# Performance work log

Measured on AMD Instinct MI355X. Metric: run time of the kernel, lower is better.

Reference implementation:

```python
import jax, jax.numpy as jnp
import numpy as np

B, T, N, H = 256, 128, 512, 128  # batch, timesteps, input_size (driving series), hidden


def setup_inputs() -> dict:
    key = jax.random.key(0)
    ks = jax.random.split(key, 7)
    p = lambda k, shape: (jax.random.normal(k, shape, dtype=jnp.float32) * 0.05)
    return {
        "X": jax.random.normal(ks[0], (B, T, N), dtype=jnp.float32),
        # attention linear: in_features = 2H + T, out_features = 1 (stored as a vector + scalar bias)
        "attn_w": p(ks[1], (2 * H + T,)),
        "attn_b": p(ks[2], ()),
        # LSTM cell params, PyTorch layout/gate order (i, f, g, o)
        "w_ih": p(ks[3], (4 * H, N)),
        "w_hh": p(ks[4], (4 * H, H)),
        "b_ih": p(ks[5], (4 * H,)),
        "b_hh": p(ks[6], (4 * H,)),
    }


def reference(X, attn_w, attn_b, w_ih, w_hh, b_ih, b_hh):
    Bn, Tn, Nn = X.shape
    Hh = w_hh.shape[1]
    # split the single attention weight row into the h / s / X-row pieces of the concat
    w_h, w_s, w_x = attn_w[:Hh], attn_w[Hh:2 * Hh], attn_w[2 * Hh:]
    Xp = jnp.swapaxes(X, 1, 2)            # [B, N, T]  (X.permute(0,2,1))
    x_score = Xp @ w_x                    # [B, N], time-invariant part of attention logits

    def step(carry, x_t):                 # x_t: [B, N] = X[:, t, :]
        h, c = carry
        # logits[b,i] = w_h.h[b] + w_s.c[b] + w_x.Xp[b,i] + b  (== Linear on the concat)
        score = x_score + (h @ w_h + c @ w_s + attn_b)[:, None]   # [B, N]
        alpha = jax.nn.softmax(score, axis=1)
        x_tilde = alpha * x_t                                      # [B, N]
        gates = x_tilde @ w_ih.T + h @ w_hh.T + b_ih + b_hh        # [B, 4H]
        i, f, g, o = jnp.split(gates, 4, axis=1)
        c_new = jax.nn.sigmoid(f) * c + jax.nn.sigmoid(i) * jnp.tanh(g)
        h_new = jax.nn.sigmoid(o) * jnp.tanh(c_new)
        return (h_new, c_new), (x_tilde, h_new)

    h0 = jnp.zeros((Bn, Hh), X.dtype)
    (_, _), (Xt, Xe) = jax.lax.scan(step, (h0, h0), jnp.swapaxes(X, 0, 1))
    # scan stacks along time -> [T, B, .]; return [B, T, .]
    return jnp.swapaxes(Xt, 0, 1), jnp.swapaxes(Xe, 0, 1)
```

## Files before the change

### kernel.cpp

```cpp
#include <hip/hip_runtime.h>
#include <hip/hip_bf16.h>

#define Bb 256
#define Tt 128
#define Nn 512
#define Hh 128

typedef __attribute__((ext_vector_type(4))) float floatx4;
typedef __attribute__((ext_vector_type(8))) short short8;

__device__ __forceinline__ unsigned short f2bf(float f) {
  unsigned u = __float_as_uint(f);
  u += 0x7fffu + ((u >> 16) & 1u);
  return (unsigned short)(u >> 16);
}

__device__ __forceinline__ float sigmoid_fast(float x) {
  return __builtin_amdgcn_rcpf(1.f + __expf(-x));
}
__device__ __forceinline__ float tanh_fast(float x) {
  float e = __expf(2.f * x);
  return 1.f - 2.f * __builtin_amdgcn_rcpf(e + 1.f);
}

__device__ __forceinline__ void lds_barrier() {
  asm volatile("s_waitcnt lgkmcnt(0)" ::: "memory");
  __builtin_amdgcn_s_barrier();
  asm volatile("" ::: "memory");
}

__global__ void prep_kernel(const float* __restrict__ w_ih,
                            const float* __restrict__ b_ih,
                            const float* __restrict__ b_hh,
                            unsigned short* __restrict__ wb,
                            float* __restrict__ bias) {
  int i = blockIdx.x * 256 + threadIdx.x;
  if (i < 4 * Hh * Nn) wb[i] = f2bf(w_ih[i]);
  if (i < 4 * Hh) bias[i] = b_ih[i] + b_hh[i];
}

__global__ __launch_bounds__(512) void alpha_kernel(const float* __restrict__ X,
                                                    const float* __restrict__ attn_w,
                                                    float* __restrict__ alpha) {
  int b = blockIdx.x;
  int n = threadIdx.x;
  const float* Xb = X + (size_t)b * Tt * Nn + n;
  float acc = 0.f;
#pragma unroll 8
  for (int t = 0; t < Tt; ++t)
    acc = fmaf(Xb[(size_t)t * Nn], attn_w[2 * Hh + t], acc);

  __shared__ float red[512];
  red[n] = acc;
  __syncthreads();
  for (int s = 256; s > 0; s >>= 1) {
    if (n < s) red[n] = fmaxf(red[n], red[n + s]);
    __syncthreads();
  }
  float m = red[0];
  __syncthreads();
  float e = __expf(acc - m);
  red[n] = e;
  __syncthreads();
  for (int s = 256; s > 0; s >>= 1) {
    if (n < s) red[n] += red[n + s];
    __syncthreads();
  }
  alpha[(size_t)b * Nn + n] = e / red[0];
}

__global__ __launch_bounds__(256) void scale_kernel(const float* __restrict__ X,
                                                    const float* __restrict__ alpha,
                                                    float* __restrict__ Xt,
                                                    unsigned short* __restrict__ xtb) {
  size_t i = (size_t)blockIdx.x * 256 + threadIdx.x;
  size_t e = i * 4;
  int n = (int)(e & (Nn - 1));
  int brow = (int)(e >> 9);
  int b = brow >> 7;
  float4 x = ((const float4*)X)[i];
  float4 a = *(const float4*)(alpha + (size_t)b * Nn + n);
  float4 y;
  y.x = x.x * a.x; y.y = x.y * a.y; y.z = x.z * a.z; y.w = x.w * a.w;
  ((float4*)Xt)[i] = y;
  ushort4 u;
  u.x = f2bf(y.x); u.y = f2bf(y.y); u.z = f2bf(y.z); u.w = f2bf(y.w);
  ((ushort4*)xtb)[i] = u;
}

#define GBK 64
#define LDK 72

__global__ __launch_bounds__(256) void gemm_bt(const unsigned short* __restrict__ A,
                                               const unsigned short* __restrict__ Bw,
                                               const float* __restrict__ bias,
                                               float* __restrict__ C) {
  __shared__ __align__(16) unsigned short As[128 * LDK];
  __shared__ __align__(16) unsigned short Bs[128 * LDK];
  const int K = 512, NO = 512;
  int tid = threadIdx.x;
  int lane = tid & 63;
  int wave = tid >> 6;
  int wm = wave & 1, wn = wave >> 1;
  int l15 = lane & 15;
  int quad = lane >> 4;
  int mtile = blockIdx.x, ntile = blockIdx.y;

  floatx4 acc[4][4];
#pragma unroll
  for (int i = 0; i < 4; ++i)
#pragma unroll
    for (int j = 0; j < 4; ++j) acc[i][j] = (floatx4){0.f, 0.f, 0.f, 0.f};

  const size_t abase = (size_t)mtile * 128 * K;
  const size_t bbase = (size_t)ntile * 128 * K;

  for (int kb = 0; kb < K; kb += GBK) {
#pragma unroll
    for (int s = 0; s < 4; ++s) {
      int idx = s * 256 + tid;
      int r = idx >> 3;
      int c = (idx & 7) * 8;
      uint4 va = *(const uint4*)(A + abase + (size_t)r * K + kb + c);
      *(uint4*)(&As[r * LDK + c]) = va;
      uint4 vb = *(const uint4*)(Bw + bbase + (size_t)r * K + kb + c);
      *(uint4*)(&Bs[r * LDK + c]) = vb;
    }
    __syncthreads();
#pragma unroll
    for (int ks = 0; ks < GBK; ks += 32) {
      int kof = ks + quad * 8;
      short8 af[4], bf[4];
#pragma unroll
      for (int i = 0; i < 4; ++i)
        af[i] = *(const short8*)(&As[(wm * 64 + i * 16 + l15) * LDK + kof]);
#pragma unroll
      for (int j = 0; j < 4; ++j)
        bf[j] = *(const short8*)(&Bs[(wn * 64 + j * 16 + l15) * LDK + kof]);
#pragma unroll
      for (int i = 0; i < 4; ++i)
#pragma unroll
        for (int j = 0; j < 4; ++j)
          acc[i][j] = __builtin_amdgcn_mfma_f32_16x16x32_bf16(af[i], bf[j], acc[i][j], 0, 0, 0);
    }
    __syncthreads();
  }

  int m0 = mtile * 128 + wm * 64;
  int n0 = ntile * 128 + wn * 64;
#pragma unroll
  for (int j = 0; j < 4; ++j) {
    int col = n0 + j * 16 + l15;
    float bsum = bias[col];
#pragma unroll
    for (int i = 0; i < 4; ++i) {
      int row = m0 + i * 16 + quad * 4;
#pragma unroll
      for (int r = 0; r < 4; ++r)
        C[(size_t)(row + r) * NO + col] = acc[i][j][r] + bsum;
    }
  }
}

__global__ __launch_bounds__(256, 1) void lstm_kernel(const float* __restrict__ G,
                                                      const float* __restrict__ w_hh,
                                                      float* __restrict__ Xe) {
  int b = blockIdx.x;
  int tid = threadIdx.x;
  int w = tid >> 6;
  int lane = tid & 63;
  int l15 = lane & 15;
  int quad = lane >> 4;

  short8 bfr[8][4];
#pragma unroll
  for (int f = 0; f < 8; ++f) {
    int ftype = f >> 1, half = f & 1;
    int n = ftype * 128 + w * 32 + half * 16 + l15;
    const float* src = w_hh + (size_t)n * 128;
#pragma unroll
    for (int kf = 0; kf < 4; ++kf) {
      int k0 = kf * 32 + quad * 8;
      float4 lo = *(const float4*)(src + k0);
      float4 hi = *(const float4*)(src + k0 + 4);
      short8 v;
      v[0] = (short)f2bf(lo.x); v[1] = (short)f2bf(lo.y);
      v[2] = (short)f2bf(lo.z); v[3] = (short)f2bf(lo.w);
      v[4] = (short)f2bf(hi.x); v[5] = (short)f2bf(hi.y);
      v[6] = (short)f2bf(hi.z); v[7] = (short)f2bf(hi.w);
      bfr[f][kf] = v;
    }
  }

  __shared__ __align__(16) unsigned short h_sh[2][128];
  if (tid < 128) h_sh[0][tid] = 0;
  __syncthreads();

  const float* Gb = G + (size_t)b * Tt * 512;
  float* Xeb = Xe + (size_t)b * Tt * Hh;

  int goff[8];
#pragma unroll
  for (int f = 0; f < 8; ++f) {
    int ftype = f >> 1, half = f & 1;
    goff[f] = ftype * 128 + w * 32 + half * 16 + l15;
  }

  float gcur[8], gnext[8];
#pragma unroll
  for (int f = 0; f < 8; ++f) gcur[f] = Gb[goff[f]];
#pragma unroll
  for (int f = 0; f < 8; ++f) gnext[f] = Gb[512 + goff[f]];

  float c0 = 0.f, c1 = 0.f;
  int j0 = w * 32 + l15;

  for (int t = 0; t < Tt; ++t) {
    int cur = t & 1;
    const unsigned short* hp = h_sh[cur];
    short8 af[4];
#pragma unroll
    for (int kf = 0; kf < 4; ++kf)
      af[kf] = *(const short8*)(hp + kf * 32 + quad * 8);

    floatx4 acc[8];
#pragma unroll
    for (int f = 0; f < 8; ++f)
      acc[f] = (floatx4){gcur[f], gcur[f], gcur[f], gcur[f]};

#pragma unroll
    for (int f = 0; f < 8; ++f) gcur[f] = gnext[f];
    if (t + 2 < Tt) {
      const float* Gt2 = Gb + (size_t)(t + 2) * 512;
#pragma unroll
      for (int f = 0; f < 8; ++f) gnext[f] = Gt2[goff[f]];
    }

#pragma unroll
    for (int kf = 0; kf < 4; ++kf)
#pragma unroll
      for (int f = 0; f < 8; ++f)
        acc[f] = __builtin_amdgcn_mfma_f32_16x16x32_bf16(af[kf], bfr[f][kf], acc[f], 0, 0, 0);

    float si0 = sigmoid_fast(acc[0][0]), si1 = sigmoid_fast(acc[1][0]);
    float sf0 = sigmoid_fast(acc[2][0]), sf1 = sigmoid_fast(acc[3][0]);
    float tg0 = tanh_fast(acc[4][0]),    tg1 = tanh_fast(acc[5][0]);
    float so0 = sigmoid_fast(acc[6][0]), so1 = sigmoid_fast(acc[7][0]);

    c0 = sf0 * c0 + si0 * tg0;
    c1 = sf1 * c1 + si1 * tg1;
    float hv0 = so0 * tanh_fast(c0);
    float hv1 = so1 * tanh_fast(c1);

    if (quad == 0) {
      float* xo = Xeb + (size_t)t * Hh;
      xo[j0] = hv0;
      xo[j0 + 16] = hv1;
      unsigned short* hn = h_sh[cur ^ 1];
      hn[j0] = f2bf(hv0);
      hn[j0 + 16] = f2bf(hv1);
    }
    lds_barrier();
  }
}

extern "C" void kernel_launch(void* const* d_in, const int* in_sizes, int n_in,
                              void* d_out, int out_size, void* d_ws, size_t ws_size,
                              hipStream_t stream) {
  const float* X      = (const float*)d_in[0];
  const float* attn_w = (const float*)d_in[1];
  const float* w_ih   = (const float*)d_in[3];
  const float* w_hh   = (const float*)d_in[4];
  const float* b_ih   = (const float*)d_in[5];
  const float* b_hh   = (const float*)d_in[6];

  float* Xt = (float*)d_out;
  float* Xe = (float*)d_out + (size_t)Bb * Tt * Nn;

  char* ws = (char*)d_ws;
  float*          alpha = (float*)(ws);
  float*          bias  = (float*)(ws + 524288);
  unsigned short* wb    = (unsigned short*)(ws + 526336);
  unsigned short* xtb   = (unsigned short*)(ws + 1050624);
  float*          G     = (float*)(ws + 34605056);

  prep_kernel<<<dim3(1024), dim3(256), 0, stream>>>(w_ih, b_ih, b_hh, wb, bias);
  alpha_kernel<<<dim3(Bb), dim3(512), 0, stream>>>(X, attn_w, alpha);
  scale_kernel<<<dim3(16384), dim3(256), 0, stream>>>(X, alpha, Xt, xtb);
  gemm_bt<<<dim3(256, 4), dim3(256), 0, stream>>>(xtb, wb, bias, G);
  lstm_kernel<<<dim3(Bb), dim3(512 / 2), 0, stream>>>(G, w_hh, Xe);
}
```

Before: 290.0 us.

## Use async global-to-LDS swizzled loads in GEMM and widen LSTM to 8 waves

The bf16 GEMM now stages tiles with global_load_lds direct-to-LDS transfers into an unpadded, XOR-swizzled layout instead of register round-trip copies into padded rows, aiming to cut load instructions and LDS bank conflicts. The LSTM recurrence kernel is widened from 256 to 512 threads, so each wave owns 16 hidden units and 4 gate MFMAs per step instead of 8. This shortens each wave's serial per-step chain and splits the weight registers across more waves. The cost is a barrier across more waves every timestep.

```diff
diff --git a/kernel.cpp b/kernel.cpp
--- a/kernel.cpp
+++ b/kernel.cpp
@@ -27,6 +27,12 @@
   asm volatile("s_waitcnt lgkmcnt(0)" ::: "memory");
   __builtin_amdgcn_s_barrier();
   asm volatile("" ::: "memory");
+}
+
+__device__ __forceinline__ void async_load16(const void* g, void* lds) {
+  __builtin_amdgcn_global_load_lds(
+      (const __attribute__((address_space(1))) unsigned int*)g,
+      (__attribute__((address_space(3))) unsigned int*)lds, 16, 0, 0);
 }
 
 __global__ void prep_kernel(const float* __restrict__ w_ih,
@@ -89,14 +95,13 @@
 }
 
 #define GBK 64
-#define LDK 72
 
 __global__ __launch_bounds__(256) void gemm_bt(const unsigned short* __restrict__ A,
                                                const unsigned short* __restrict__ Bw,
                                                const float* __restrict__ bias,
                                                float* __restrict__ C) {
-  __shared__ __align__(16) unsigned short As[128 * LDK];
-  __shared__ __align__(16) unsigned short Bs[128 * LDK];
+  __shared__ __align__(16) unsigned short As[128 * 64];
+  __shared__ __align__(16) unsigned short Bs[128 * 64];
   const int K = 512, NO = 512;
   int tid = threadIdx.x;
   int lane = tid & 63;
@@ -112,31 +117,31 @@
 #pragma unroll
     for (int j = 0; j < 4; ++j) acc[i][j] = (floatx4){0.f, 0.f, 0.f, 0.f};
 
-  const size_t abase = (size_t)mtile * 128 * K;
-  const size_t bbase = (size_t)ntile * 128 * K;
+  int lr = lane >> 3;
+  int lc = (lane & 7) ^ lr;
+  const size_t lane_goff = (size_t)lr * K + lc * 8;
+  const size_t abase = (size_t)mtile * 128 * K + lane_goff;
+  const size_t bbase = (size_t)ntile * 128 * K + lane_goff;
+  int sw = (quad ^ (l15 & 7)) * 8;
 
   for (int kb = 0; kb < K; kb += GBK) {
 #pragma unroll
-    for (int s = 0; s < 4; ++s) {
-      int idx = s * 256 + tid;
-      int r = idx >> 3;
-      int c = (idx & 7) * 8;
-      uint4 va = *(const uint4*)(A + abase + (size_t)r * K + kb + c);
-      *(uint4*)(&As[r * LDK + c]) = va;
-      uint4 vb = *(const uint4*)(Bw + bbase + (size_t)r * K + kb + c);
-      *(uint4*)(&Bs[r * LDK + c]) = vb;
-    }
-    __syncthreads();
-#pragma unroll
-    for (int ks = 0; ks < GBK; ks += 32) {
-      int kof = ks + quad * 8;
+    for (int slot = 0; slot < 4; ++slot) {
+      int r0 = slot * 32 + wave * 8;
+      async_load16(A + abase + (size_t)r0 * K + kb, &As[r0 * 64]);
+      async_load16(Bw + bbase + (size_t)r0 * K + kb, &Bs[r0 * 64]);
+    }
+    __syncthreads();
+#pragma unroll
+    for (int kh = 0; kh < 2; ++kh) {
+      int sc = sw ^ (kh * 32);
       short8 af[4], bf[4];
 #pragma unroll
       for (int i = 0; i < 4; ++i)
-        af[i] = *(const short8*)(&As[(wm * 64 + i * 16 + l15) * LDK + kof]);
+        af[i] = *(const short8*)(&As[(wm * 64 + i * 16 + l15) * 64 + sc]);
 #pragma unroll
       for (int j = 0; j < 4; ++j)
-        bf[j] = *(const short8*)(&Bs[(wn * 64 + j * 16 + l15) * LDK + kof]);
+        bf[j] = *(const short8*)(&Bs[(wn * 64 + j * 16 + l15) * 64 + sc]);
 #pragma unroll
       for (int i = 0; i < 4; ++i)
 #pragma unroll
@@ -162,7 +167,7 @@
   }
 }
 
-__global__ __launch_bounds__(256, 1) void lstm_kernel(const float* __restrict__ G,
+__global__ __launch_bounds__(512, 1) void lstm_kernel(const float* __restrict__ G,
                                                       const float* __restrict__ w_hh,
                                                       float* __restrict__ Xe) {
   int b = blockIdx.x;
@@ -172,11 +177,10 @@
   int l15 = lane & 15;
   int quad = lane >> 4;
 
-  short8 bfr[8][4];
-#pragma unroll
-  for (int f = 0; f < 8; ++f) {
-    int ftype = f >> 1, half = f & 1;
-    int n = ftype * 128 + w * 32 + half * 16 + l15;
+  short8 bfr[4][4];
+#pragma unroll
+  for (int f = 0; f < 4; ++f) {
+    int n = f * 128 + w * 16 + l15;
     const float* src = w_hh + (size_t)n * 128;
 #pragma unroll
     for (int kf = 0; kf < 4; ++kf) {
@@ -199,21 +203,18 @@
   const float* Gb = G + (size_t)b * Tt * 512;
   float* Xeb = Xe + (size_t)b * Tt * Hh;
 
-  int goff[8];
-#pragma unroll
-  for (int f = 0; f < 8; ++f) {
-    int ftype = f >> 1, half = f & 1;
-    goff[f] = ftype * 128 + w * 32 + half * 16 + l15;
-  }
-
-  float gcur[8], gnext[8];
-#pragma unroll
-  for (int f = 0; f < 8; ++f) gcur[f] = Gb[goff[f]];
-#pragma unroll
-  for (int f = 0; f < 8; ++f) gnext[f] = Gb[512 + goff[f]];
-
-  float c0 = 0.f, c1 = 0.f;
-  int j0 = w * 32 + l15;
+  int goff[4];
+#pragma unroll
+  for (int f = 0; f < 4; ++f) goff[f] = f * 128 + w * 16 + l15;
+
+  float gcur[4], gnext[4];
+#pragma unroll
+  for (int f = 0; f < 4; ++f) gcur[f] = Gb[goff[f]];
+#pragma unroll
+  for (int f = 0; f < 4; ++f) gnext[f] = Gb[512 + goff[f]];
+
+  float c0 = 0.f;
+  int j0 = w * 16 + l15;
 
   for (int t = 0; t < Tt; ++t) {
     int cur = t & 1;
@@ -223,42 +224,36 @@
     for (int kf = 0; kf < 4; ++kf)
       af[kf] = *(const short8*)(hp + kf * 32 + quad * 8);
 
-    floatx4 acc[8];
-#pragma unroll
-    for (int f = 0; f < 8; ++f)
+    floatx4 acc[4];
+#pragma unroll
+    for (int f = 0; f < 4; ++f)
       acc[f] = (floatx4){gcur[f], gcur[f], gcur[f], gcur[f]};
 
 #pragma unroll
-    for (int f = 0; f < 8; ++f) gcur[f] = gnext[f];
+    for (int f = 0; f < 4; ++f) gcur[f] = gnext[f];
     if (t + 2 < Tt) {
       const float* Gt2 = Gb + (size_t)(t + 2) * 512;
 #pragma unroll
-      for (int f = 0; f < 8; ++f) gnext[f] = Gt2[goff[f]];
+      for (int f = 0; f < 4; ++f) gnext[f] = Gt2[goff[f]];
     }
 
 #pragma unroll
     for (int kf = 0; kf < 4; ++kf)
 #pragma unroll
-      for (int f = 0; f < 8; ++f)
+      for (int f = 0; f < 4; ++f)
         acc[f] = __builtin_amdgcn_mfma_f32_16x16x32_bf16(af[kf], bfr[f][kf], acc[f], 0, 0, 0);
 
-    float si0 = sigmoid_fast(acc[0][0]), si1 = sigmoid_fast(acc[1][0]);
-    float sf0 = sigmoid_fast(acc[2][0]), sf1 = sigmoid_fast(acc[3][0]);
-    float tg0 = tanh_fast(acc[4][0]),    tg1 = tanh_fast(acc[5][0]);
-    float so0 = sigmoid_fast(acc[6][0]), so1 = sigmoid_fast(acc[7][0]);
-
-    c0 = sf0 * c0 + si0 * tg0;
-    c1 = sf1 * c1 + si1 * tg1;
-    float hv0 = so0 * tanh_fast(c0);
-    float hv1 = so1 * tanh_fast(c1);
+    float si = sigmoid_fast(acc[0][0]);
+    float sf = sigmoid_fast(acc[1][0]);
+    float tg = tanh_fast(acc[2][0]);
+    float so = sigmoid_fast(acc[3][0]);
+
+    c0 = sf * c0 + si * tg;
+    float hv = so * tanh_fast(c0);
 
     if (quad == 0) {
-      float* xo = Xeb + (size_t)t * Hh;
-      xo[j0] = hv0;
-      xo[j0 + 16] = hv1;
-      unsigned short* hn = h_sh[cur ^ 1];
-      hn[j0] = f2bf(hv0);
-      hn[j0 + 16] = f2bf(hv1);
+      Xeb[(size_t)t * Hh + j0] = hv;
+      h_sh[cur ^ 1][j0] = f2bf(hv);
     }
     lds_barrier();
   }
@@ -288,5 +283,5 @@
   alpha_kernel<<<dim3(Bb), dim3(512), 0, stream>>>(X, attn_w, alpha);
   scale_kernel<<<dim3(16384), dim3(256), 0, stream>>>(X, alpha, Xt, xtb);
   gemm_bt<<<dim3(256, 4), dim3(256), 0, stream>>>(xtb, wb, bias, G);
-  lstm_kernel<<<dim3(Bb), dim3(512 / 2), 0, stream>>>(G, w_hh, Xe);
-}
+  lstm_kernel<<<dim3(Bb), dim3(512), 0, stream>>>(G, w_hh, Xe);
+}
```

New measurement: 275.1 us. 5.1% less time.
